# Kernel tuning notes

Measured on AMD Instinct MI355X. Metric: run time of the kernel, lower is better.

Reference implementation:

```python
import jax, jax.numpy as jnp
import numpy as np

A = 2048        # atoms
D = 64          # depth (in_depth == out_depth)
FL = 12         # filter_length


def setup_inputs() -> dict:
    key = jax.random.key(0)
    k = jax.random.split(key, 7)
    return {
        "x": jax.random.normal(k[0], (A, D), dtype=jnp.float32),
        "connectivity": jax.random.uniform(k[1], (A, A, FL), dtype=jnp.float32),
        "bond_property": jax.random.normal(k[2], (A, FL, 2), dtype=jnp.float32),
        "pf0": jax.random.normal(k[3], (D, FL, D), dtype=jnp.float32) * 0.01,
        "bf0": jax.random.normal(k[4], (D, FL, 3), dtype=jnp.float32) * 0.01,
        "pf1": jax.random.normal(k[5], (D, FL, D), dtype=jnp.float32) * 0.01,
        "bf1": jax.random.normal(k[6], (D, FL, 3), dtype=jnp.float32) * 0.01,
    }


def _chem_conv(h, connectivity, bond_property, pf, bf):
    # h: (A, D); connectivity: (A, A_src, FL); pf: (O, FL, D); bf: (O, FL, 3)
    # node_connection[a,f,d] = sum_k connectivity[a,k,f] * h[k,d]
    node_conn = jnp.einsum('akf,kd->afd', connectivity, h)
    # bond_score[a,o,f] = sum_d node_conn[a,f,d] * pf[o,f,d]
    score = jnp.einsum('afd,ofd->aof', node_conn, pf)
    # combined = cat([score, bond_property], -1); out = sum over (f, 3) of combined * bf
    out = (jnp.einsum('aof,of->ao', score, bf[:, :, 0])
           + jnp.einsum('afc,ofc->ao', bond_property, bf[:, :, 1:3]))
    return out  # (A, O)


def reference(x, connectivity, bond_property, pf0, bf0, pf1, bf1):
    act = jax.nn.relu
    out = x
    for pf, bf in ((pf0, bf0), (pf1, bf1)):
        out = act(_chem_conv(out, connectivity, bond_property, pf, bf))
        out = _chem_conv(out, connectivity, bond_property, pf, bf) + x
        out = act(out)
    return out
```

## Files before the change

kernel.cpp:

```cpp
#include <hip/hip_runtime.h>
#include <hip/hip_bf16.h>

#define A_N   2048
#define D_N   64
#define FL_N  12
#define KTOT  (A_N * FL_N)
#define S_SPLIT 16
#define KCHUNK 1536
#define NBK   12
#define TILE_B 16384

typedef __attribute__((ext_vector_type(8))) short bf16x8;
typedef __attribute__((ext_vector_type(4))) short bf16x4;
typedef __attribute__((ext_vector_type(4))) float f32x4;

__device__ __forceinline__ short f2bf(float f) {
  union { __hip_bfloat16 b; short s; } u;
  u.b = __float2bfloat16(f);
  return u.s;
}

__device__ __forceinline__ void gload16(const void* g, void* l) {
  __builtin_amdgcn_global_load_lds(
      (const __attribute__((address_space(1))) unsigned int*)g,
      (__attribute__((address_space(3))) unsigned int*)l, 16, 0, 0);
}

__global__ void k_setup_cvt(const float* __restrict__ pf0, const float* __restrict__ bf0,
                            const float* __restrict__ pf1, const float* __restrict__ bf1,
                            const float* __restrict__ bp, const float* __restrict__ x,
                            const float* __restrict__ conn,
                            short* __restrict__ P2_0, short* __restrict__ P2_1,
                            float* __restrict__ bond0, float* __restrict__ bond1,
                            short* __restrict__ xb, short* __restrict__ connb2) {
  int b = blockIdx.x, t = threadIdx.x;
  if (b >= 768) {
    size_t slot = (size_t)(b - 768) * 256 + t;
#pragma unroll
    for (int cc = 0; cc < 6; ++cc) {
      size_t i = (slot + (size_t)cc * 1048576) * 8;
      f32x4 a0 = __builtin_nontemporal_load((const f32x4*)(conn + i));
      f32x4 a1 = __builtin_nontemporal_load((const f32x4*)(conn + i + 4));
      bf16x8 v;
      v[0]=f2bf(a0[0]); v[1]=f2bf(a0[1]); v[2]=f2bf(a0[2]); v[3]=f2bf(a0[3]);
      v[4]=f2bf(a1[0]); v[5]=f2bf(a1[1]); v[6]=f2bf(a1[2]); v[7]=f2bf(a1[3]);
      int a = (int)(i / KTOT), c = (int)(i % KTOT);
      int rt = a >> 6, r = a & 63;
      int kc = c / KCHUNK, rem = c % KCHUNK;
      int bk = rem >> 7, k = rem & 127;
      int cw = ((k >> 3) ^ (r & 7));
      size_t dst = ((size_t)((rt * 16 + kc) * NBK + bk) << 14) + (r << 8) + (cw << 4);
      *(bf16x8*)((char*)connb2 + dst) = v;
    }
    return;
  }
  if (b < 192) {
    int idx = b * 256 + t;
    int f = (idx >> 6) % FL_N;
    int o = idx / (D_N * FL_N);
    P2_0[idx] = f2bf(pf0[idx] * bf0[(o * FL_N + f) * 3]);
    P2_1[idx] = f2bf(pf1[idx] * bf1[(o * FL_N + f) * 3]);
  } else if (b < 704) {
    int o = t & 63;
    int a = (b - 192) * 4 + (t >> 6);
    float s0 = 0.f, s1 = 0.f;
#pragma unroll
    for (int f = 0; f < FL_N; ++f) {
      float c0 = bp[(a * FL_N + f) * 2 + 0];
      float c1 = bp[(a * FL_N + f) * 2 + 1];
      s0 += c0 * bf0[(o * FL_N + f) * 3 + 1] + c1 * bf0[(o * FL_N + f) * 3 + 2];
      s1 += c0 * bf1[(o * FL_N + f) * 3 + 1] + c1 * bf1[(o * FL_N + f) * 3 + 2];
    }
    bond0[a * D_N + o] = s0;
    bond1[a * D_N + o] = s1;
  } else {
    int i = ((b - 704) * 256 + t) * 8;
    f32x4 a0 = *(const f32x4*)(x + i);
    f32x4 a1 = *(const f32x4*)(x + i + 4);
    bf16x8 v;
    v[0]=f2bf(a0[0]); v[1]=f2bf(a0[1]); v[2]=f2bf(a0[2]); v[3]=f2bf(a0[3]);
    v[4]=f2bf(a1[0]); v[5]=f2bf(a1[1]); v[6]=f2bf(a1[2]); v[7]=f2bf(a1[3]);
    *(bf16x8*)(xb + i) = v;
  }
}

__device__ __forceinline__ void prep_body(bf16x8 h0, bf16x8 h1,
                                          const short* __restrict__ P2,
                                          short* __restrict__ Bt2,
                                          int k0, int lane, int w) {
  int l15 = lane & 15, grp = lane >> 4;
  const short* prow = P2 + (w * 16 + l15) * (FL_N * D_N) + grp * 8;
  f32x4 acc[FL_N];
#pragma unroll
  for (int f = 0; f < FL_N; ++f) {
    bf16x8 p0 = *(const bf16x8*)(prow + f * D_N);
    bf16x8 p1 = *(const bf16x8*)(prow + f * D_N + 32);
    f32x4 c = {0.f, 0.f, 0.f, 0.f};
    c = __builtin_amdgcn_mfma_f32_16x16x32_bf16(p0, h0, c, 0, 0, 0);
    c = __builtin_amdgcn_mfma_f32_16x16x32_bf16(p1, h1, c, 0, 0, 0);
    acc[f] = c;
  }
#pragma unroll
  for (int r = 0; r < 4; ++r) {
    int o = w * 16 + grp * 4 + r;
    int katom = k0 + l15;
#pragma unroll
    for (int f = 0; f < FL_N; ++f) {
      int c = katom * FL_N + f;
      int kc = c / KCHUNK, rem = c % KCHUNK;
      int bk = rem >> 7, kk = rem & 127;
      int cw = ((kk >> 3) ^ (o & 7));
      *(short*)((char*)Bt2 + ((size_t)(kc * NBK + bk) << 14)
                + (o << 8) + (cw << 4) + ((kk & 7) << 1))
          = f2bf(acc[f][r]);
    }
  }
}

__global__ void k_prep0(const short* __restrict__ xb, const short* __restrict__ P2,
                        short* __restrict__ Bt2) {
  int lane = threadIdx.x & 63, w = threadIdx.x >> 6;
  int l15 = lane & 15, grp = lane >> 4;
  int k0 = blockIdx.x * 16;
  const short* hrow = xb + (k0 + l15) * D_N + grp * 8;
  bf16x8 h0 = *(const bf16x8*)(hrow);
  bf16x8 h1 = *(const bf16x8*)(hrow + 32);
  prep_body(h0, h1, P2, Bt2, k0, lane, w);
}

template <int ADDX>
__global__ void k_prep_r(const float* __restrict__ part, const float* __restrict__ bond,
                         const float* __restrict__ x, const short* __restrict__ P2,
                         short* __restrict__ Bt2) {
  __shared__ short hsh[16 * 64];
  int t = threadIdx.x;
  int k0 = blockIdx.x * 16;
  int r  = t >> 4;
  int d0 = (t & 15) * 4;
  size_t base = (size_t)(k0 + r) * D_N + d0;
  f32x4 s = *(const f32x4*)(bond + base);
#pragma unroll
  for (int si = 0; si < S_SPLIT; ++si) {
    f32x4 p = *(const f32x4*)(part + (size_t)si * (A_N * D_N) + base);
    s[0] += p[0]; s[1] += p[1]; s[2] += p[2]; s[3] += p[3];
  }
  if (ADDX) {
    f32x4 xv = *(const f32x4*)(x + base);
    s[0] += xv[0]; s[1] += xv[1]; s[2] += xv[2]; s[3] += xv[3];
  }
  bf16x4 hv;
  hv[0] = f2bf(fmaxf(s[0], 0.f)); hv[1] = f2bf(fmaxf(s[1], 0.f));
  hv[2] = f2bf(fmaxf(s[2], 0.f)); hv[3] = f2bf(fmaxf(s[3], 0.f));
  *(bf16x4*)(&hsh[r * 64 + d0]) = hv;
  __syncthreads();
  int lane = t & 63, w = t >> 6, l15 = lane & 15, grp = lane >> 4;
  bf16x8 h0 = *(const bf16x8*)(&hsh[l15 * 64 + grp * 8]);
  bf16x8 h1 = *(const bf16x8*)(&hsh[l15 * 64 + grp * 8 + 32]);
  prep_body(h0, h1, P2, Bt2, k0, lane, w);
}

template <int C>
__global__ __launch_bounds__(256, 2) void k_gemm(const short* __restrict__ connb2,
                                                 const short* __restrict__ Bt2,
                                                 float* __restrict__ part) {
  __shared__ short lA[2][8192];
  __shared__ short lB[2][8192];
  int t = threadIdx.x;
  int lane = t & 63, w = t >> 6, l15 = lane & 15, grp = lane >> 4;
  int rt = blockIdx.x, kc = blockIdx.y;

  const char* Ab = (const char*)connb2 + (((size_t)(rt * 16 + kc) * NBK) << 14);
  const char* Bb = (const char*)Bt2 + (((size_t)kc * NBK) << 14);
  const int wq = w << 10;
  const int lane16 = lane << 4;

#pragma unroll
  for (int q = 0; q < 4; ++q) {
    gload16(Ab + q * 4096 + wq + lane16, (char*)&lA[0][0] + q * 4096 + wq);
    gload16(Bb + q * 4096 + wq + lane16, (char*)&lB[0][0] + q * 4096 + wq);
  }
  __syncthreads();

  f32x4 acc0 = {0,0,0,0}, acc1 = {0,0,0,0}, acc2 = {0,0,0,0}, acc3 = {0,0,0,0};
  const int arow = (w * 16 + l15) << 8;
  const int brow = l15 << 8;
  const int key  = (l15 & 7) << 4;

#pragma unroll
  for (int bk = 0; bk < NBK; ++bk) {
    const int cur = bk & 1;
    const int nxt = cur ^ 1;
    if (bk + 1 < NBK) {
      const char* An = Ab + (size_t)(bk + 1) * TILE_B;
      const char* Bn = Bb + (size_t)(bk + 1) * TILE_B;
#pragma unroll
      for (int q = 0; q < 4; ++q) {
        gload16(An + q * 4096 + wq + lane16, (char*)&lA[nxt][0] + q * 4096 + wq);
        gload16(Bn + q * 4096 + wq + lane16, (char*)&lB[nxt][0] + q * 4096 + wq);
      }
    }
    const char* la = (const char*)&lA[cur][0];
    const char* lb = (const char*)&lB[cur][0];
#pragma unroll
    for (int ks = 0; ks < 4; ++ks) {
      const int cb = ((ks << 6) + (grp << 4)) ^ key;
      bf16x8 af = *(const bf16x8*)(la + arow + cb);
      bf16x8 b0 = *(const bf16x8*)(lb + brow + cb);
      bf16x8 b1 = *(const bf16x8*)(lb + 4096 + brow + cb);
      bf16x8 b2 = *(const bf16x8*)(lb + 8192 + brow + cb);
      bf16x8 b3 = *(const bf16x8*)(lb + 12288 + brow + cb);
      acc0 = __builtin_amdgcn_mfma_f32_16x16x32_bf16(af, b0, acc0, 0, 0, 0);
      acc1 = __builtin_amdgcn_mfma_f32_16x16x32_bf16(af, b1, acc1, 0, 0, 0);
      acc2 = __builtin_amdgcn_mfma_f32_16x16x32_bf16(af, b2, acc2, 0, 0, 0);
      acc3 = __builtin_amdgcn_mfma_f32_16x16x32_bf16(af, b3, acc3, 0, 0, 0);
    }
    if (bk + 1 < NBK) __syncthreads();
  }

  float* p = part + (size_t)kc * (A_N * D_N);
  int rbase = rt * 64 + w * 16 + grp * 4;
#pragma unroll
  for (int r = 0; r < 4; ++r) {
    float* pr = p + (size_t)(rbase + r) * D_N + l15;
    pr[0]  = acc0[r];
    pr[16] = acc1[r];
    pr[32] = acc2[r];
    pr[48] = acc3[r];
  }
}

__global__ void k_final(const float* __restrict__ part, const float* __restrict__ bond,
                        const float* __restrict__ x, float* __restrict__ out) {
  int i = blockIdx.x * 256 + threadIdx.x;
  float s = bond[i];
#pragma unroll
  for (int si = 0; si < S_SPLIT; ++si) s += part[(size_t)si * (A_N * D_N) + i];
  out[i] = fmaxf(s + x[i], 0.f);
}

extern "C" void kernel_launch(void* const* d_in, const int* in_sizes, int n_in,
                              void* d_out, int out_size, void* d_ws, size_t ws_size,
                              hipStream_t stream) {
  const float* x    = (const float*)d_in[0];
  const float* conn = (const float*)d_in[1];
  const float* bprp = (const float*)d_in[2];
  const float* pf0  = (const float*)d_in[3];
  const float* bf0  = (const float*)d_in[4];
  const float* pf1  = (const float*)d_in[5];
  const float* bf1  = (const float*)d_in[6];
  float* out = (float*)d_out;

  char* ws = (char*)d_ws;
  size_t off = 0;
  short* connb2 = (short*)(ws + off); off += (size_t)A_N * KTOT * 2;
  short* Bt2    = (short*)(ws + off); off += (size_t)D_N * KTOT * 2;
  float* part   = (float*)(ws + off); off += (size_t)S_SPLIT * A_N * D_N * 4;
  short* xb     = (short*)(ws + off); off += (size_t)A_N * D_N * 2;
  float* bond0  = (float*)(ws + off); off += (size_t)A_N * D_N * 4;
  float* bond1  = (float*)(ws + off); off += (size_t)A_N * D_N * 4;
  short* P2_0   = (short*)(ws + off); off += (size_t)D_N * FL_N * D_N * 2;
  short* P2_1   = (short*)(ws + off); off += (size_t)D_N * FL_N * D_N * 2;

  k_setup_cvt<<<4864, 256, 0, stream>>>(pf0, bf0, pf1, bf1, bprp, x, conn,
                                        P2_0, P2_1, bond0, bond1, xb, connb2);

  dim3 ggrid(32, S_SPLIT);

  k_prep0<<<128, 256, 0, stream>>>(xb, P2_0, Bt2);
  k_gemm<0><<<ggrid, 256, 0, stream>>>(connb2, Bt2, part);

  k_prep_r<0><<<128, 256, 0, stream>>>(part, bond0, x, P2_0, Bt2);
  k_gemm<1><<<ggrid, 256, 0, stream>>>(connb2, Bt2, part);

  k_prep_r<1><<<128, 256, 0, stream>>>(part, bond0, x, P2_1, Bt2);
  k_gemm<2><<<ggrid, 256, 0, stream>>>(connb2, Bt2, part);

  k_prep_r<0><<<128, 256, 0, stream>>>(part, bond1, x, P2_1, Bt2);
  k_gemm<3><<<ggrid, 256, 0, stream>>>(connb2, Bt2, part);

  k_final<<<512, 256, 0, stream>>>(part, bond1, x, out);
}
```

Measured before the change: 185.8 us.

## Load GEMM A-operand directly to registers and double split-K chunks

```diff
diff --git a/kernel.cpp b/kernel.cpp
--- a/kernel.cpp
+++ b/kernel.cpp
@@ -5,9 +5,9 @@
 #define D_N   64
 #define FL_N  12
 #define KTOT  (A_N * FL_N)
-#define S_SPLIT 16
-#define KCHUNK 1536
-#define NBK   12
+#define S_SPLIT 32
+#define KCHUNK 768
+#define NBK   6
 #define TILE_B 16384
 
 typedef __attribute__((ext_vector_type(8))) short bf16x8;
@@ -49,7 +49,7 @@
       int kc = c / KCHUNK, rem = c % KCHUNK;
       int bk = rem >> 7, k = rem & 127;
       int cw = ((k >> 3) ^ (r & 7));
-      size_t dst = ((size_t)((rt * 16 + kc) * NBK + bk) << 14) + (r << 8) + (cw << 4);
+      size_t dst = ((size_t)((rt * S_SPLIT + kc) * NBK + bk) << 14) + (r << 8) + (cw << 4);
       *(bf16x8*)((char*)connb2 + dst) = v;
     }
     return;
@@ -160,31 +160,35 @@
 }
 
 template <int C>
-__global__ __launch_bounds__(256, 2) void k_gemm(const short* __restrict__ connb2,
+__global__ __launch_bounds__(256, 4) void k_gemm(const short* __restrict__ connb2,
                                                  const short* __restrict__ Bt2,
                                                  float* __restrict__ part) {
-  __shared__ short lA[2][8192];
   __shared__ short lB[2][8192];
   int t = threadIdx.x;
   int lane = t & 63, w = t >> 6, l15 = lane & 15, grp = lane >> 4;
   int rt = blockIdx.x, kc = blockIdx.y;
 
-  const char* Ab = (const char*)connb2 + (((size_t)(rt * 16 + kc) * NBK) << 14);
+  const char* Ab = (const char*)connb2 + (((size_t)(rt * S_SPLIT + kc) * NBK) << 14);
   const char* Bb = (const char*)Bt2 + (((size_t)kc * NBK) << 14);
   const int wq = w << 10;
   const int lane16 = lane << 4;
-
-#pragma unroll
-  for (int q = 0; q < 4; ++q) {
-    gload16(Ab + q * 4096 + wq + lane16, (char*)&lA[0][0] + q * 4096 + wq);
+  const int key = (l15 & 7) << 4;
+
+  int aoff[4];
+#pragma unroll
+  for (int ks = 0; ks < 4; ++ks)
+    aoff[ks] = ((w * 16 + l15) << 8) + (((ks << 6) + (grp << 4)) ^ key);
+
+#pragma unroll
+  for (int q = 0; q < 4; ++q)
     gload16(Bb + q * 4096 + wq + lane16, (char*)&lB[0][0] + q * 4096 + wq);
-  }
+  bf16x8 a[2][4];
+#pragma unroll
+  for (int ks = 0; ks < 4; ++ks) a[0][ks] = *(const bf16x8*)(Ab + aoff[ks]);
   __syncthreads();
 
   f32x4 acc0 = {0,0,0,0}, acc1 = {0,0,0,0}, acc2 = {0,0,0,0}, acc3 = {0,0,0,0};
-  const int arow = (w * 16 + l15) << 8;
   const int brow = l15 << 8;
-  const int key  = (l15 & 7) << 4;
 
 #pragma unroll
   for (int bk = 0; bk < NBK; ++bk) {
@@ -194,25 +198,23 @@
       const char* An = Ab + (size_t)(bk + 1) * TILE_B;
       const char* Bn = Bb + (size_t)(bk + 1) * TILE_B;
 #pragma unroll
-      for (int q = 0; q < 4; ++q) {
-        gload16(An + q * 4096 + wq + lane16, (char*)&lA[nxt][0] + q * 4096 + wq);
+      for (int q = 0; q < 4; ++q)
         gload16(Bn + q * 4096 + wq + lane16, (char*)&lB[nxt][0] + q * 4096 + wq);
-      }
-    }
-    const char* la = (const char*)&lA[cur][0];
+#pragma unroll
+      for (int ks = 0; ks < 4; ++ks) a[nxt][ks] = *(const bf16x8*)(An + aoff[ks]);
+    }
     const char* lb = (const char*)&lB[cur][0];
 #pragma unroll
     for (int ks = 0; ks < 4; ++ks) {
       const int cb = ((ks << 6) + (grp << 4)) ^ key;
-      bf16x8 af = *(const bf16x8*)(la + arow + cb);
       bf16x8 b0 = *(const bf16x8*)(lb + brow + cb);
       bf16x8 b1 = *(const bf16x8*)(lb + 4096 + brow + cb);
       bf16x8 b2 = *(const bf16x8*)(lb + 8192 + brow + cb);
       bf16x8 b3 = *(const bf16x8*)(lb + 12288 + brow + cb);
-      acc0 = __builtin_amdgcn_mfma_f32_16x16x32_bf16(af, b0, acc0, 0, 0, 0);
-      acc1 = __builtin_amdgcn_mfma_f32_16x16x32_bf16(af, b1, acc1, 0, 0, 0);
-      acc2 = __builtin_amdgcn_mfma_f32_16x16x32_bf16(af, b2, acc2, 0, 0, 0);
-      acc3 = __builtin_amdgcn_mfma_f32_16x16x32_bf16(af, b3, acc3, 0, 0, 0);
+      acc0 = __builtin_amdgcn_mfma_f32_16x16x32_bf16(a[cur][ks], b0, acc0, 0, 0, 0);
+      acc1 = __builtin_amdgcn_mfma_f32_16x16x32_bf16(a[cur][ks], b1, acc1, 0, 0, 0);
+      acc2 = __builtin_amdgcn_mfma_f32_16x16x32_bf16(a[cur][ks], b2, acc2, 0, 0, 0);
+      acc3 = __builtin_amdgcn_mfma_f32_16x16x32_bf16(a[cur][ks], b3, acc3, 0, 0, 0);
     }
     if (bk + 1 < NBK) __syncthreads();
   }
```

New measurement: 189.3 us. Within noise of the previous version (+1.9%).
